# Kernel tuning notes

Measured on AMD Instinct MI355X. Metric: run time of the kernel, lower is better.

Reference implementation:

```python
import jax, jax.numpy as jnp
import numpy as np

NUM_NODES = 15000


def _gcn_conv(x, W, b, src, dst, norm, num_nodes):
    # PyG GCNConv: x' = D^-1/2 (A + I) D^-1/2 (x W) + b
    h = x @ W                                   # [N, out]
    msg = h[src] * norm[:, None]                # gather + scale per edge
    out = jax.ops.segment_sum(msg, dst, num_segments=num_nodes)
    return out + b


def setup_inputs() -> dict:
    key = jax.random.key(0)
    ks = jax.random.split(key, 12)
    T = 100000
    E = 200000
    inp = {
        "x": jax.random.normal(ks[0], (NUM_NODES, 768), jnp.float32),
        "r_emb": jax.random.normal(ks[1], (T, 768), jnp.float32),
        "W1": jax.random.normal(ks[2], (768, 10), jnp.float32) * 0.05,
        "b1": jax.random.normal(ks[3], (10,), jnp.float32) * 0.05,
        "W2": jax.random.normal(ks[4], (10, 128), jnp.float32) * 0.05,
        "b2": jax.random.normal(ks[5], (128,), jnp.float32) * 0.05,
        "W_ih": jax.random.normal(ks[6], (512, 1024), jnp.float32) * 0.03,
        "W_hh": jax.random.normal(ks[7], (512, 128), jnp.float32) * 0.03,
        "b_ih": jax.random.normal(ks[8], (512,), jnp.float32) * 0.03,
        "b_hh": jax.random.normal(ks[9], (512,), jnp.float32) * 0.03,
        "edge_index": jax.random.randint(ks[10], (2, E), 0, NUM_NODES).astype(jnp.int64),
        "triples": jax.random.randint(ks[11], (T, 3), 0, NUM_NODES).astype(jnp.int64),
    }
    return inp


def reference(x, r_emb, W1, b1, W2, b2, W_ih, W_hh, b_ih, b_hh, edge_index, triples):
    N = x.shape[0]
    H = 128  # lstm hidden size
    # --- add self loops, symmetric GCN normalization ---
    loop = jnp.arange(N, dtype=edge_index.dtype)
    src = jnp.concatenate([edge_index[0], loop])
    dst = jnp.concatenate([edge_index[1], loop])
    deg = jax.ops.segment_sum(jnp.ones_like(dst, jnp.float32), dst, num_segments=N)
    dinv = jnp.where(deg > 0, jax.lax.rsqrt(deg), 0.0)
    norm = dinv[src] * dinv[dst]                      # [E+N]
    # --- 2-layer GCN ---
    h = jax.nn.relu(_gcn_conv(x, W1, b1, src, dst, norm, N))   # [N, 10]
    z = _gcn_conv(h, W2, b2, src, dst, norm, N)                # [N, 128]
    # --- per-triple LSTM scoring, batched (seq_len=1, zero init state) ---
    hvec = z[triples[:, 0]]                           # [T, 128]
    tvec = z[triples[:, 2]]                           # [T, 128]
    feat = jnp.concatenate([hvec, r_emb, tvec], axis=-1)       # [T, 1024]
    gates = feat @ W_ih.T + (b_ih + b_hh)             # [T, 512]; h0=0 so W_hh term vanishes
    i_g, f_g, g_g, o_g = jnp.split(gates, 4, axis=-1)  # torch gate order i,f,g,o
    c = jax.nn.sigmoid(i_g) * jnp.tanh(g_g)           # c0 = 0 -> forget term drops
    out = jax.nn.sigmoid(o_g) * jnp.tanh(c)           # [T, 128]
    score = jax.nn.sigmoid(jnp.sum(out, axis=-1))     # [T]
    return score
```

## Files before the change

### kernel.cpp

```cpp
#include <hip/hip_runtime.h>

#define NF 768
#define D1 10
#define D2 128
#define BM 64
#define NS 24

typedef __attribute__((ext_vector_type(8))) short bf16x8;
typedef __attribute__((ext_vector_type(16))) float f32x16;

static __device__ __forceinline__ float sigf(float v){ return 1.0f/(1.0f+__expf(-v)); }
static __device__ __forceinline__ float tanhfast(float v){ return 2.0f/(1.0f+__expf(-2.0f*v)) - 1.0f; }
static __device__ __forceinline__ short f2bf(float f){
    unsigned u = __float_as_uint(f);
    u += 0x7fffu + ((u>>16)&1u);
    return (short)(u>>16);
}
static __device__ __forceinline__ float bf2f(ushort h){
    return __uint_as_float(((unsigned)h)<<16);
}

__global__ void k_deg(const int* __restrict__ dst, int* __restrict__ cnt, int E){
    int e = blockIdx.x*256 + threadIdx.x;
    if(e<E) atomicAdd(&cnt[dst[e]], 1);
}
__global__ void k_dinv(const int* __restrict__ cnt, float* __restrict__ dinv, int N){
    int n = blockIdx.x*256 + threadIdx.x;
    if(n<N) dinv[n] = rsqrtf((float)cnt[n] + 1.0f);
}

__global__ __launch_bounds__(256) void k_scan(const int* __restrict__ cnt,
                                              int* __restrict__ rowptr,
                                              int* __restrict__ rowcur, int N, int E){
    __shared__ int part[256];
    int t = threadIdx.x;
    int C = (N+255)/256;
    int lo = t*C, hi = lo+C; if(hi>N) hi=N; if(lo>N) lo=N;
    int s=0;
    for(int i=lo;i<hi;i++) s += cnt[i];
    part[t]=s;
    __syncthreads();
    if(t==0){
        int run=0;
        for(int i=0;i<256;i++){ int v=part[i]; part[i]=run; run+=v; }
        rowptr[N]=E;
    }
    __syncthreads();
    int run = part[t];
    for(int i=lo;i<hi;i++){ rowptr[i]=run; rowcur[i]=run; run += cnt[i]; }
}

__global__ void k_fill(const int* __restrict__ src, const int* __restrict__ dst,
                       const float* __restrict__ dinv, int* __restrict__ rowcur,
                       int* __restrict__ esrc, float* __restrict__ enorm, int E){
    int e = blockIdx.x*256 + threadIdx.x;
    if(e>=E) return;
    int s=src[e], d=dst[e];
    int pos = atomicAdd(&rowcur[d], 1);
    esrc[pos]=s;
    enorm[pos]=dinv[s]*dinv[d];
}

__global__ __launch_bounds__(256) void k_h1(const float* __restrict__ x,
                                            const float* __restrict__ W1,
                                            float* __restrict__ h1, int N){
    __shared__ float w1s[NF*D1];
    for(int i=threadIdx.x;i<NF*D1;i+=256) w1s[i]=W1[i];
    __syncthreads();
    int row = blockIdx.x*4 + (threadIdx.x>>6);
    int lane = threadIdx.x&63;
    if(row>=N) return;
    const float* xr = x + (size_t)row*NF;
    float acc[D1];
#pragma unroll
    for(int c=0;c<D1;c++) acc[c]=0.f;
#pragma unroll
    for(int i=0;i<NF/64;i++){
        float xa = xr[lane+64*i];
        const float* w = &w1s[(lane+64*i)*D1];
#pragma unroll
        for(int c=0;c<D1;c++) acc[c] += xa*w[c];
    }
#pragma unroll
    for(int c=0;c<D1;c++){
        float v=acc[c];
#pragma unroll
        for(int off=32;off;off>>=1) v += __shfl_down(v,off,64);
        if(lane==0) h1[(size_t)row*D1+c]=v;
    }
}

__global__ void k_scat1(const int* __restrict__ src, const int* __restrict__ dst,
                        const float* __restrict__ dinv, const float* __restrict__ h1,
                        float* __restrict__ agg1, int E){
    int gid = blockIdx.x*256 + threadIdx.x;
    if(gid >= E*D1) return;
    int e = gid/D1, c = gid - e*D1;
    int s = src[e], d = dst[e];
    float norm = dinv[s]*dinv[d];
    atomicAdd(&agg1[(size_t)d*D1+c], h1[(size_t)s*D1+c]*norm);
}

__global__ void k_relu(float* __restrict__ agg1, const float* __restrict__ h1,
                       const float* __restrict__ dinv, const float* __restrict__ b1, int N){
    int gid = blockIdx.x*256 + threadIdx.x;
    if(gid >= N*D1) return;
    int n = gid/D1, c = gid - n*D1;
    float di = dinv[n];
    float v = agg1[gid] + h1[gid]*di*di + b1[c];
    agg1[gid] = v>0.f ? v : 0.f;
}

__global__ __launch_bounds__(128) void k_hz(const float* __restrict__ h,
                                            const float* __restrict__ W2,
                                            float* __restrict__ hz, int N){
    __shared__ float w2s[D1*D2];
    int j = threadIdx.x;
    for(int i=j;i<D1*D2;i+=128) w2s[i]=W2[i];
    __syncthreads();
    int n = blockIdx.x;
    if(n>=N) return;
    const float* hr = h + (size_t)n*D1;
    float acc=0.f;
#pragma unroll
    for(int k=0;k<D1;k++) acc += hr[k]*w2s[k*D2+j];
    hz[(size_t)n*D2+j]=acc;
}

__global__ __launch_bounds__(128) void k_gath2(const float* __restrict__ hz,
        const int* __restrict__ rowptr, const int* __restrict__ esrc,
        const float* __restrict__ enorm, const float* __restrict__ dinv,
        const float* __restrict__ b2, float* __restrict__ z, int N){
    int n = blockIdx.x;
    int c = threadIdx.x;
    int e0 = rowptr[n], e1 = rowptr[n+1];
    float di = dinv[n];
    float acc = hz[(size_t)n*D2+c]*di*di + b2[c];
    int e = e0;
    for(; e+1<e1; e+=2){
        int s0=esrc[e], s1=esrc[e+1];
        float w0=enorm[e], w1=enorm[e+1];
        acc += hz[(size_t)s0*D2+c]*w0 + hz[(size_t)s1*D2+c]*w1;
    }
    if(e<e1) acc += hz[(size_t)esrc[e]*D2+c]*enorm[e];
    z[(size_t)n*D2+c]=acc;
}

__global__ void k_wimgB(const float* __restrict__ Wih, ushort* __restrict__ img){
    int gid = blockIdx.x*256 + threadIdx.x;
    if(gid >= 12*48*64) return;
    int l = gid & 63;
    int ks16 = (gid>>6) % 48;
    int f = gid / (48*64);
    int dd = l & 31, kb = l>>5;
    int wn = f/3, gi = f - wn*3;
    int gbase = (gi==0)?0:((gi==1)?256:384);
    int wrow = gbase + wn*32 + dd;
    int k = ks16*16 + kb*8;
    const float* p = Wih + (size_t)wrow*1024 + 128 + k;
    float4 v0=*(const float4*)p, v1=*(const float4*)(p+4);
    bf16x8 o;
    o[0]=f2bf(v0.x); o[1]=f2bf(v0.y); o[2]=f2bf(v0.z); o[3]=f2bf(v0.w);
    o[4]=f2bf(v1.x); o[5]=f2bf(v1.y); o[6]=f2bf(v1.z); o[7]=f2bf(v1.w);
    *(bf16x8*)(img + (size_t)gid*8) = o;
}

__global__ void k_wimgZ(const float* __restrict__ Wih, ushort* __restrict__ img){
    int gid = blockIdx.x*256 + threadIdx.x;
    if(gid >= 24*8*64) return;
    int l = gid & 63;
    int ks16 = (gid>>6) & 7;
    int f = gid >> 9;
    int j = f*32 + (l&31);
    int kb = l>>5;
    int k = ks16*16 + kb*8;
    int jq = (j<384)? j : j-384;
    int wrow = (jq<128)? jq : jq+128;
    int wcol = (j<384)? k : (896+k);
    const float* p = Wih + (size_t)wrow*1024 + wcol;
    float4 v0=*(const float4*)p, v1=*(const float4*)(p+4);
    bf16x8 o;
    o[0]=f2bf(v0.x); o[1]=f2bf(v0.y); o[2]=f2bf(v0.z); o[3]=f2bf(v0.w);
    o[4]=f2bf(v1.x); o[5]=f2bf(v1.y); o[6]=f2bf(v1.z); o[7]=f2bf(v1.w);
    *(bf16x8*)(img + (size_t)gid*8) = o;
}

__global__ __launch_bounds__(256) void k_zw_m(const float* __restrict__ z,
                                              const ushort* __restrict__ img,
                                              ushort* __restrict__ zwht, int N){
    __shared__ ushort As[8*64*8];
    int tid=threadIdx.x, lane=tid&63, w=tid>>6;
    int n0 = blockIdx.x*32;
#pragma unroll
    for(int i=0;i<2;i++){
        int s = tid + 256*i;
        int ks16 = s>>6, l = s&63;
        int row = l&31, kb=l>>5;
        int n = n0+row; if(n>=N) n=N-1;
        const float* p = z + (size_t)n*D2 + ks16*16 + kb*8;
        float4 v0=*(const float4*)p, v1=*(const float4*)(p+4);
        bf16x8 o;
        o[0]=f2bf(v0.x); o[1]=f2bf(v0.y); o[2]=f2bf(v0.z); o[3]=f2bf(v0.w);
        o[4]=f2bf(v1.x); o[5]=f2bf(v1.y); o[6]=f2bf(v1.z); o[7]=f2bf(v1.w);
        *(bf16x8*)(&As[(size_t)s*8]) = o;
    }
    __syncthreads();
    f32x16 acc[6];
    const f32x16 zer = {0,0,0,0,0,0,0,0,0,0,0,0,0,0,0,0};
#pragma unroll
    for(int nf=0;nf<6;nf++) acc[nf]=zer;
#pragma unroll
    for(int ks16=0;ks16<8;ks16++){
        bf16x8 a = *(const bf16x8*)&As[(ks16*64+lane)*8];
#pragma unroll
        for(int nf=0;nf<6;nf++){
            int f = w*6+nf;
            bf16x8 b = *(const bf16x8*)(img + ((size_t)(f*8+ks16)*64 + lane)*8);
            acc[nf] = __builtin_amdgcn_mfma_f32_32x32x16_bf16(a,b,acc[nf],0,0,0);
        }
    }
    int l31=lane&31, lh=lane>>5;
#pragma unroll
    for(int nf=0;nf<6;nf++){
        int j = (w*6+nf)*32 + l31;
#pragma unroll
        for(int r=0;r<16;r++){
            int row = (r&3)+8*(r>>2)+4*lh;
            int n = n0+row;
            if(n<N) zwht[(size_t)n*768 + j] = (ushort)f2bf(acc[nf][r]);
        }
    }
}

__global__ __launch_bounds__(256,3) void k_big(
    const float* __restrict__ remb, const ushort* __restrict__ img,
    const ushort* __restrict__ zwht, const float* __restrict__ b_ih,
    const float* __restrict__ b_hh, const int* __restrict__ trip,
    float* __restrict__ score, int T)
{
    __shared__ ushort As[2][4*64*8];
    __shared__ float rowsum[BM];
    __shared__ int sh_th[BM], sh_tt[BM];
    int tid=threadIdx.x, lane=tid&63, wn=tid>>6;
    int l31=lane&31, lh=lane>>5;
    int t0 = blockIdx.x*BM;
    if(tid<BM){
        rowsum[tid]=0.f;
        int t=t0+tid, tc=(t<T)?t:T-1;
        sh_th[tid]=trip[3*tc]; sh_tt[tid]=trip[3*tc+2];
    }
    const int arow=(tid&7)+8*(tid>>5);
    const int akb=(tid>>3)&1, akh=(tid>>4)&1;
    const int aslot = (((arow>>5)*2+akh)*64 + (arow&31)+32*akb)*8;
    const size_t arowg = (size_t)((t0+arow<T)?(t0+arow):(T-1))*NF + akb*8 + akh*16;
    const ushort* wbase = img + ((size_t)(wn*3)*48*64 + lane)*8;

    float4 p0a,p0b,p1a,p1b;
    p0a=*(const float4*)(remb+arowg);      p0b=*(const float4*)(remb+arowg+4);
    p1a=*(const float4*)(remb+arowg+32);   p1b=*(const float4*)(remb+arowg+36);

    f32x16 acc[2][3];
    const f32x16 zer = {0,0,0,0,0,0,0,0,0,0,0,0,0,0,0,0};
#pragma unroll
    for(int m=0;m<2;m++)
#pragma unroll
        for(int g=0;g<3;g++) acc[m][g]=zer;

#define STAGE(B,VA,VB) { bf16x8 o_; \
    o_[0]=f2bf(VA.x); o_[1]=f2bf(VA.y); o_[2]=f2bf(VA.z); o_[3]=f2bf(VA.w); \
    o_[4]=f2bf(VB.x); o_[5]=f2bf(VB.y); o_[6]=f2bf(VB.z); o_[7]=f2bf(VB.w); \
    *(bf16x8*)(&As[B][aslot]) = o_; }

#define COMPUTE(B,KS) { \
    _Pragma("unroll") \
    for(int kh=0;kh<2;kh++){ \
        bf16x8 a0 = *(const bf16x8*)&As[B][((0*2+kh)*64+lane)*8]; \
        bf16x8 a1 = *(const bf16x8*)&As[B][((1*2+kh)*64+lane)*8]; \
        int ksh = (KS)*2+kh; \
        bf16x8 b0 = *(const bf16x8*)(wbase + (size_t)(0*48+ksh)*512); \
        bf16x8 b1 = *(const bf16x8*)(wbase + (size_t)(1*48+ksh)*512); \
        bf16x8 b2v= *(const bf16x8*)(wbase + (size_t)(2*48+ksh)*512); \
        acc[0][0]=__builtin_amdgcn_mfma_f32_32x32x16_bf16(a0,b0 ,acc[0][0],0,0,0); \
        acc[0][1]=__builtin_amdgcn_mfma_f32_32x32x16_bf16(a0,b1 ,acc[0][1],0,0,0); \
        acc[0][2]=__builtin_amdgcn_mfma_f32_32x32x16_bf16(a0,b2v,acc[0][2],0,0,0); \
        acc[1][0]=__builtin_amdgcn_mfma_f32_32x32x16_bf16(a1,b0 ,acc[1][0],0,0,0); \
        acc[1][1]=__builtin_amdgcn_mfma_f32_32x32x16_bf16(a1,b1 ,acc[1][1],0,0,0); \
        acc[1][2]=__builtin_amdgcn_mfma_f32_32x32x16_bf16(a1,b2v,acc[1][2],0,0,0); \
    } }

    STAGE(0, p0a, p0b);
    __syncthreads();

    for(int ks=0; ks<NS; ks+=2){
        if(ks+2<NS){
            p0a=*(const float4*)(remb+arowg+(size_t)(ks+2)*32);
            p0b=*(const float4*)(remb+arowg+(size_t)(ks+2)*32+4);
        }
        STAGE(1, p1a, p1b);
        COMPUTE(0, ks);
        __syncthreads();
        if(ks+3<NS){
            p1a=*(const float4*)(remb+arowg+(size_t)(ks+3)*32);
            p1b=*(const float4*)(remb+arowg+(size_t)(ks+3)*32+4);
        }
        if(ks+2<NS){ STAGE(0, p0a, p0b); }
        COMPUTE(1, ks+1);
        __syncthreads();
    }

    int d = wn*32+l31;
    float bi=b_ih[d]+b_hh[d];
    float bg=b_ih[256+d]+b_hh[256+d];
    float bo=b_ih[384+d]+b_hh[384+d];
#pragma unroll
    for(int m=0;m<2;m++){
#pragma unroll
        for(int r=0;r<16;r++){
            int row = m*32 + (r&3)+8*(r>>2)+4*lh;
            int t = t0+row;
            float ov = 0.f;
            if(t<T){
                const ushort* zh = zwht + (size_t)sh_th[row]*768;
                const ushort* zt = zwht + (size_t)sh_tt[row]*768 + 384;
                float ig = acc[m][0][r] + bf2f(zh[d])     + bf2f(zt[d])     + bi;
                float gg = acc[m][1][r] + bf2f(zh[128+d]) + bf2f(zt[128+d]) + bg;
                float og = acc[m][2][r] + bf2f(zh[256+d]) + bf2f(zt[256+d]) + bo;
                float cc = sigf(ig)*tanhfast(gg);
                ov = sigf(og)*tanhfast(cc);
            }
#pragma unroll
            for(int off=1; off<32; off<<=1) ov += __shfl_xor(ov, off, 64);
            if(l31==0) atomicAdd(&rowsum[row], ov);
        }
    }
    __syncthreads();
    if(tid < BM){
        int t = t0 + tid;
        if(t < T) score[t] = sigf(rowsum[tid]);
    }
#undef STAGE
#undef COMPUTE
}

extern "C" void kernel_launch(void* const* d_in, const int* in_sizes, int n_in,
                              void* d_out, int out_size, void* d_ws, size_t ws_size,
                              hipStream_t stream){
    const float* x    = (const float*)d_in[0];
    const float* remb = (const float*)d_in[1];
    const float* W1   = (const float*)d_in[2];
    const float* b1   = (const float*)d_in[3];
    const float* W2   = (const float*)d_in[4];
    const float* b2   = (const float*)d_in[5];
    const float* Wih  = (const float*)d_in[6];
    const float* b_ih = (const float*)d_in[8];
    const float* b_hh = (const float*)d_in[9];
    const int*   ei   = (const int*)d_in[10];
    const int*   trip = (const int*)d_in[11];
    float* score = (float*)d_out;

    const int N = in_sizes[0]/NF;
    const int E = in_sizes[10]/2;
    const int T = in_sizes[11]/3;
    const int* src = ei;
    const int* dst = ei + E;

    float* ws = (float*)d_ws;
    size_t o = 0;
    ushort* WimgB = (ushort*)(ws+o); o += 12*48*64*8/2;
    ushort* WimgZ = (ushort*)(ws+o); o += 24*8*64*8/2;
    ushort* zwht  = (ushort*)(ws+o); o += (size_t)N*768/2;
    int*   cnt    = (int*)(ws+o);    o += (size_t)((N+8)&~7);
    int*   rowptr = (int*)(ws+o);    o += (size_t)((N+8)&~7);
    int*   rowcur = (int*)(ws+o);    o += (size_t)((N+8)&~7);
    int*   esrc   = (int*)(ws+o);    o += (size_t)E;
    float* enorm  = ws+o;            o += (size_t)E;
    float* dinv   = ws+o;            o += (size_t)((N+7)&~7);
    float* h1     = ws+o;            o += (size_t)N*D1;
    float* agg1   = ws+o;            o += (size_t)N*D1;
    float* hz     = ws+o;            o += (size_t)N*D2;
    float* z      = ws+o;            o += (size_t)N*D2;
    (void)ws_size; (void)n_in; (void)out_size;

    hipMemsetAsync(cnt, 0, (size_t)N*sizeof(int), stream);
    hipMemsetAsync(agg1, 0, (size_t)N*D1*sizeof(float), stream);

    k_wimgB<<<dim3((12*48*64+255)/256), dim3(256), 0, stream>>>(Wih, WimgB);
    k_wimgZ<<<dim3((24*8*64+255)/256),  dim3(256), 0, stream>>>(Wih, WimgZ);
    k_deg  <<<dim3((E+255)/256), dim3(256), 0, stream>>>(dst, cnt, E);
    k_dinv <<<dim3((N+255)/256), dim3(256), 0, stream>>>(cnt, dinv, N);
    k_scan <<<dim3(1), dim3(256), 0, stream>>>(cnt, rowptr, rowcur, N, E);
    k_fill <<<dim3((E+255)/256), dim3(256), 0, stream>>>(src, dst, dinv, rowcur, esrc, enorm, E);
    k_h1   <<<dim3((N+3)/4), dim3(256), 0, stream>>>(x, W1, h1, N);
    k_scat1<<<dim3((E*D1+255)/256), dim3(256), 0, stream>>>(src, dst, dinv, h1, agg1, E);
    k_relu <<<dim3((N*D1+255)/256), dim3(256), 0, stream>>>(agg1, h1, dinv, b1, N);
    k_hz   <<<dim3(N), dim3(128), 0, stream>>>(agg1, W2, hz, N);
    k_gath2<<<dim3(N), dim3(128), 0, stream>>>(hz, rowptr, esrc, enorm, dinv, b2, z, N);
    k_zw_m <<<dim3((N+31)/32), dim3(256), 0, stream>>>(z, WimgZ, zwht, N);
    k_big  <<<dim3((T+BM-1)/BM), dim3(256), 0, stream>>>(remb, WimgB, zwht, b_ih, b_hh, trip, score, T);
}
```

Baseline: 363.0 us.

## Fold z·W_ih head/tail projection into main MFMA GEMM and restructure GCN layer one

The precomputed per-node z·W_ih table (k_zw_m, k_wimgZ) is removed. The main triple kernel now gathers bf16 z rows for head and tail and runs them as extra K-steps in its MFMA GEMM over the full 1024-wide input. That GEMM no longer stages through LDS: each lane loads A fragments directly from global memory into a register-prefetch pipeline, and __launch_bounds__ drops the occupancy hint. Layer one's atomic scatter plus ReLU pass is replaced by a CSR gather kernel, dinv is folded into the scan, and k_h1 reads x as float4 against a transposed W1. This removes the large zwht intermediate and several launches, at the cost of extra per-triple MFMA work and uncoalesced direct global A-fragment loads.

```diff
diff --git a/kernel.cpp b/kernel.cpp
--- a/kernel.cpp
+++ b/kernel.cpp
@@ -4,7 +4,6 @@
 #define D1 10
 #define D2 128
 #define BM 64
-#define NS 24
 
 typedef __attribute__((ext_vector_type(8))) short bf16x8;
 typedef __attribute__((ext_vector_type(16))) float f32x16;
@@ -16,22 +15,15 @@
     u += 0x7fffu + ((u>>16)&1u);
     return (short)(u>>16);
 }
-static __device__ __forceinline__ float bf2f(ushort h){
-    return __uint_as_float(((unsigned)h)<<16);
-}
 
 __global__ void k_deg(const int* __restrict__ dst, int* __restrict__ cnt, int E){
     int e = blockIdx.x*256 + threadIdx.x;
     if(e<E) atomicAdd(&cnt[dst[e]], 1);
 }
-__global__ void k_dinv(const int* __restrict__ cnt, float* __restrict__ dinv, int N){
-    int n = blockIdx.x*256 + threadIdx.x;
-    if(n<N) dinv[n] = rsqrtf((float)cnt[n] + 1.0f);
-}
 
 __global__ __launch_bounds__(256) void k_scan(const int* __restrict__ cnt,
-                                              int* __restrict__ rowptr,
-                                              int* __restrict__ rowcur, int N, int E){
+                                              int* __restrict__ rowptr, int* __restrict__ rowcur,
+                                              float* __restrict__ dinv, int N, int E){
     __shared__ int part[256];
     int t = threadIdx.x;
     int C = (N+255)/256;
@@ -47,7 +39,10 @@
     }
     __syncthreads();
     int run = part[t];
-    for(int i=lo;i<hi;i++){ rowptr[i]=run; rowcur[i]=run; run += cnt[i]; }
+    for(int i=lo;i<hi;i++){
+        rowptr[i]=run; rowcur[i]=run; run += cnt[i];
+        dinv[i] = rsqrtf((float)cnt[i] + 1.0f);
+    }
 }
 
 __global__ void k_fill(const int* __restrict__ src, const int* __restrict__ dst,
@@ -64,51 +59,78 @@
 __global__ __launch_bounds__(256) void k_h1(const float* __restrict__ x,
                                             const float* __restrict__ W1,
                                             float* __restrict__ h1, int N){
-    __shared__ float w1s[NF*D1];
-    for(int i=threadIdx.x;i<NF*D1;i+=256) w1s[i]=W1[i];
+    __shared__ float wt[D1*NF];
+    for(int idx=threadIdx.x; idx<NF*D1; idx+=256){
+        int k=idx/D1, c=idx-k*D1;
+        wt[c*NF+k]=W1[idx];
+    }
     __syncthreads();
     int row = blockIdx.x*4 + (threadIdx.x>>6);
     int lane = threadIdx.x&63;
     if(row>=N) return;
-    const float* xr = x + (size_t)row*NF;
+    const float4* xr = (const float4*)(x + (size_t)row*NF);
     float acc[D1];
 #pragma unroll
     for(int c=0;c<D1;c++) acc[c]=0.f;
 #pragma unroll
-    for(int i=0;i<NF/64;i++){
-        float xa = xr[lane+64*i];
-        const float* w = &w1s[(lane+64*i)*D1];
-#pragma unroll
-        for(int c=0;c<D1;c++) acc[c] += xa*w[c];
+    for(int i=0;i<3;i++){
+        float4 v = xr[lane + 64*i];
+#pragma unroll
+        for(int c=0;c<D1;c++){
+            float4 w = *(const float4*)&wt[c*NF + (lane+64*i)*4];
+            acc[c] += v.x*w.x + v.y*w.y + v.z*w.z + v.w*w.w;
+        }
     }
 #pragma unroll
     for(int c=0;c<D1;c++){
         float v=acc[c];
 #pragma unroll
         for(int off=32;off;off>>=1) v += __shfl_down(v,off,64);
-        if(lane==0) h1[(size_t)row*D1+c]=v;
-    }
-}
-
-__global__ void k_scat1(const int* __restrict__ src, const int* __restrict__ dst,
-                        const float* __restrict__ dinv, const float* __restrict__ h1,
-                        float* __restrict__ agg1, int E){
-    int gid = blockIdx.x*256 + threadIdx.x;
-    if(gid >= E*D1) return;
-    int e = gid/D1, c = gid - e*D1;
-    int s = src[e], d = dst[e];
-    float norm = dinv[s]*dinv[d];
-    atomicAdd(&agg1[(size_t)d*D1+c], h1[(size_t)s*D1+c]*norm);
-}
-
-__global__ void k_relu(float* __restrict__ agg1, const float* __restrict__ h1,
-                       const float* __restrict__ dinv, const float* __restrict__ b1, int N){
-    int gid = blockIdx.x*256 + threadIdx.x;
-    if(gid >= N*D1) return;
-    int n = gid/D1, c = gid - n*D1;
-    float di = dinv[n];
-    float v = agg1[gid] + h1[gid]*di*di + b1[c];
-    agg1[gid] = v>0.f ? v : 0.f;
+        acc[c]=v;
+    }
+    if(lane==0){
+#pragma unroll
+        for(int c=0;c<D1;c++) h1[(size_t)row*D1+c]=acc[c];
+    }
+}
+
+__global__ __launch_bounds__(256) void k_gath1(const float* __restrict__ h1,
+        const int* __restrict__ rowptr, const int* __restrict__ esrc,
+        const float* __restrict__ enorm, const float* __restrict__ dinv,
+        const float* __restrict__ b1, float* __restrict__ h, int N){
+    int node = blockIdx.x*4 + (threadIdx.x>>6);
+    int lane = threadIdx.x&63;
+    if(node>=N) return;
+    int e0=rowptr[node], e1=rowptr[node+1];
+    float acc[D1];
+#pragma unroll
+    for(int c=0;c<D1;c++) acc[c]=0.f;
+    for(int e=e0+lane; e<e1; e+=64){
+        int s=esrc[e]; float w=enorm[e];
+        const float* hr = h1 + (size_t)s*D1;
+#pragma unroll
+        for(int c=0;c<D1;c++) acc[c] += hr[c]*w;
+    }
+    if(lane==0){
+        float di=dinv[node], d2=di*di;
+        const float* hr = h1 + (size_t)node*D1;
+#pragma unroll
+        for(int c=0;c<D1;c++) acc[c] += hr[c]*d2;
+    }
+#pragma unroll
+    for(int c=0;c<D1;c++){
+        float v=acc[c];
+#pragma unroll
+        for(int off=32;off;off>>=1) v += __shfl_down(v,off,64);
+        acc[c]=v;
+    }
+    if(lane==0){
+#pragma unroll
+        for(int c=0;c<D1;c++){
+            float v = acc[c] + b1[c];
+            h[(size_t)node*D1+c] = v>0.f ? v : 0.f;
+        }
+    }
 }
 
 __global__ __launch_bounds__(128) void k_hz(const float* __restrict__ h,
@@ -130,7 +152,7 @@
 __global__ __launch_bounds__(128) void k_gath2(const float* __restrict__ hz,
         const int* __restrict__ rowptr, const int* __restrict__ esrc,
         const float* __restrict__ enorm, const float* __restrict__ dinv,
-        const float* __restrict__ b2, float* __restrict__ z, int N){
+        const float* __restrict__ b2, ushort* __restrict__ zb, int N){
     int n = blockIdx.x;
     int c = threadIdx.x;
     int e0 = rowptr[n], e1 = rowptr[n+1];
@@ -143,21 +165,21 @@
         acc += hz[(size_t)s0*D2+c]*w0 + hz[(size_t)s1*D2+c]*w1;
     }
     if(e<e1) acc += hz[(size_t)esrc[e]*D2+c]*enorm[e];
-    z[(size_t)n*D2+c]=acc;
+    zb[(size_t)n*D2+c] = (ushort)f2bf(acc);
 }
 
 __global__ void k_wimgB(const float* __restrict__ Wih, ushort* __restrict__ img){
     int gid = blockIdx.x*256 + threadIdx.x;
-    if(gid >= 12*48*64) return;
+    if(gid >= 12*64*64) return;
     int l = gid & 63;
-    int ks16 = (gid>>6) % 48;
-    int f = gid / (48*64);
+    int ks16 = (gid>>6) & 63;
+    int f = gid >> 12;
     int dd = l & 31, kb = l>>5;
     int wn = f/3, gi = f - wn*3;
     int gbase = (gi==0)?0:((gi==1)?256:384);
     int wrow = gbase + wn*32 + dd;
     int k = ks16*16 + kb*8;
-    const float* p = Wih + (size_t)wrow*1024 + 128 + k;
+    const float* p = Wih + (size_t)wrow*1024 + k;
     float4 v0=*(const float4*)p, v1=*(const float4*)(p+4);
     bf16x8 o;
     o[0]=f2bf(v0.x); o[1]=f2bf(v0.y); o[2]=f2bf(v0.z); o[3]=f2bf(v0.w);
@@ -165,99 +187,32 @@
     *(bf16x8*)(img + (size_t)gid*8) = o;
 }
 
-__global__ void k_wimgZ(const float* __restrict__ Wih, ushort* __restrict__ img){
-    int gid = blockIdx.x*256 + threadIdx.x;
-    if(gid >= 24*8*64) return;
-    int l = gid & 63;
-    int ks16 = (gid>>6) & 7;
-    int f = gid >> 9;
-    int j = f*32 + (l&31);
-    int kb = l>>5;
-    int k = ks16*16 + kb*8;
-    int jq = (j<384)? j : j-384;
-    int wrow = (jq<128)? jq : jq+128;
-    int wcol = (j<384)? k : (896+k);
-    const float* p = Wih + (size_t)wrow*1024 + wcol;
-    float4 v0=*(const float4*)p, v1=*(const float4*)(p+4);
-    bf16x8 o;
-    o[0]=f2bf(v0.x); o[1]=f2bf(v0.y); o[2]=f2bf(v0.z); o[3]=f2bf(v0.w);
-    o[4]=f2bf(v1.x); o[5]=f2bf(v1.y); o[6]=f2bf(v1.z); o[7]=f2bf(v1.w);
-    *(bf16x8*)(img + (size_t)gid*8) = o;
-}
-
-__global__ __launch_bounds__(256) void k_zw_m(const float* __restrict__ z,
-                                              const ushort* __restrict__ img,
-                                              ushort* __restrict__ zwht, int N){
-    __shared__ ushort As[8*64*8];
-    int tid=threadIdx.x, lane=tid&63, w=tid>>6;
-    int n0 = blockIdx.x*32;
-#pragma unroll
-    for(int i=0;i<2;i++){
-        int s = tid + 256*i;
-        int ks16 = s>>6, l = s&63;
-        int row = l&31, kb=l>>5;
-        int n = n0+row; if(n>=N) n=N-1;
-        const float* p = z + (size_t)n*D2 + ks16*16 + kb*8;
-        float4 v0=*(const float4*)p, v1=*(const float4*)(p+4);
-        bf16x8 o;
-        o[0]=f2bf(v0.x); o[1]=f2bf(v0.y); o[2]=f2bf(v0.z); o[3]=f2bf(v0.w);
-        o[4]=f2bf(v1.x); o[5]=f2bf(v1.y); o[6]=f2bf(v1.z); o[7]=f2bf(v1.w);
-        *(bf16x8*)(&As[(size_t)s*8]) = o;
-    }
-    __syncthreads();
-    f32x16 acc[6];
-    const f32x16 zer = {0,0,0,0,0,0,0,0,0,0,0,0,0,0,0,0};
-#pragma unroll
-    for(int nf=0;nf<6;nf++) acc[nf]=zer;
-#pragma unroll
-    for(int ks16=0;ks16<8;ks16++){
-        bf16x8 a = *(const bf16x8*)&As[(ks16*64+lane)*8];
-#pragma unroll
-        for(int nf=0;nf<6;nf++){
-            int f = w*6+nf;
-            bf16x8 b = *(const bf16x8*)(img + ((size_t)(f*8+ks16)*64 + lane)*8);
-            acc[nf] = __builtin_amdgcn_mfma_f32_32x32x16_bf16(a,b,acc[nf],0,0,0);
-        }
-    }
-    int l31=lane&31, lh=lane>>5;
-#pragma unroll
-    for(int nf=0;nf<6;nf++){
-        int j = (w*6+nf)*32 + l31;
-#pragma unroll
-        for(int r=0;r<16;r++){
-            int row = (r&3)+8*(r>>2)+4*lh;
-            int n = n0+row;
-            if(n<N) zwht[(size_t)n*768 + j] = (ushort)f2bf(acc[nf][r]);
-        }
-    }
-}
-
-__global__ __launch_bounds__(256,3) void k_big(
+__global__ __launch_bounds__(256) void k_big(
     const float* __restrict__ remb, const ushort* __restrict__ img,
-    const ushort* __restrict__ zwht, const float* __restrict__ b_ih,
+    const ushort* __restrict__ zb, const float* __restrict__ b_ih,
     const float* __restrict__ b_hh, const int* __restrict__ trip,
     float* __restrict__ score, int T)
 {
-    __shared__ ushort As[2][4*64*8];
     __shared__ float rowsum[BM];
-    __shared__ int sh_th[BM], sh_tt[BM];
     int tid=threadIdx.x, lane=tid&63, wn=tid>>6;
     int l31=lane&31, lh=lane>>5;
-    int t0 = blockIdx.x*BM;
-    if(tid<BM){
-        rowsum[tid]=0.f;
-        int t=t0+tid, tc=(t<T)?t:T-1;
-        sh_th[tid]=trip[3*tc]; sh_tt[tid]=trip[3*tc+2];
-    }
-    const int arow=(tid&7)+8*(tid>>5);
-    const int akb=(tid>>3)&1, akh=(tid>>4)&1;
-    const int aslot = (((arow>>5)*2+akh)*64 + (arow&31)+32*akb)*8;
-    const size_t arowg = (size_t)((t0+arow<T)?(t0+arow):(T-1))*NF + akb*8 + akh*16;
-    const ushort* wbase = img + ((size_t)(wn*3)*48*64 + lane)*8;
-
-    float4 p0a,p0b,p1a,p1b;
-    p0a=*(const float4*)(remb+arowg);      p0b=*(const float4*)(remb+arowg+4);
-    p1a=*(const float4*)(remb+arowg+32);   p1b=*(const float4*)(remb+arowg+36);
+    int t0=blockIdx.x*BM;
+    if(tid<BM) rowsum[tid]=0.f;
+    __syncthreads();
+
+    int th[2], tt[2];
+    size_t rbase[2];
+#pragma unroll
+    for(int m=0;m<2;m++){
+        int t = t0 + l31 + m*32; if(t>=T) t=T-1;
+        rbase[m] = (size_t)t*NF;
+        th[m]=trip[3*t]; tt[m]=trip[3*t+2];
+    }
+    const float* ra0 = remb + rbase[0] + lh*8;
+    const float* ra1 = remb + rbase[1] + lh*8;
+    const ushort* wb0 = img + ((size_t)(wn*3+0)*64*64 + lane)*8;
+    const ushort* wb1 = img + ((size_t)(wn*3+1)*64*64 + lane)*8;
+    const ushort* wb2 = img + ((size_t)(wn*3+2)*64*64 + lane)*8;
 
     f32x16 acc[2][3];
     const f32x16 zer = {0,0,0,0,0,0,0,0,0,0,0,0,0,0,0,0};
@@ -266,47 +221,83 @@
 #pragma unroll
         for(int g=0;g<3;g++) acc[m][g]=zer;
 
-#define STAGE(B,VA,VB) { bf16x8 o_; \
-    o_[0]=f2bf(VA.x); o_[1]=f2bf(VA.y); o_[2]=f2bf(VA.z); o_[3]=f2bf(VA.w); \
-    o_[4]=f2bf(VB.x); o_[5]=f2bf(VB.y); o_[6]=f2bf(VB.z); o_[7]=f2bf(VB.w); \
-    *(bf16x8*)(&As[B][aslot]) = o_; }
-
-#define COMPUTE(B,KS) { \
-    _Pragma("unroll") \
-    for(int kh=0;kh<2;kh++){ \
-        bf16x8 a0 = *(const bf16x8*)&As[B][((0*2+kh)*64+lane)*8]; \
-        bf16x8 a1 = *(const bf16x8*)&As[B][((1*2+kh)*64+lane)*8]; \
-        int ksh = (KS)*2+kh; \
-        bf16x8 b0 = *(const bf16x8*)(wbase + (size_t)(0*48+ksh)*512); \
-        bf16x8 b1 = *(const bf16x8*)(wbase + (size_t)(1*48+ksh)*512); \
-        bf16x8 b2v= *(const bf16x8*)(wbase + (size_t)(2*48+ksh)*512); \
-        acc[0][0]=__builtin_amdgcn_mfma_f32_32x32x16_bf16(a0,b0 ,acc[0][0],0,0,0); \
-        acc[0][1]=__builtin_amdgcn_mfma_f32_32x32x16_bf16(a0,b1 ,acc[0][1],0,0,0); \
-        acc[0][2]=__builtin_amdgcn_mfma_f32_32x32x16_bf16(a0,b2v,acc[0][2],0,0,0); \
-        acc[1][0]=__builtin_amdgcn_mfma_f32_32x32x16_bf16(a1,b0 ,acc[1][0],0,0,0); \
-        acc[1][1]=__builtin_amdgcn_mfma_f32_32x32x16_bf16(a1,b1 ,acc[1][1],0,0,0); \
-        acc[1][2]=__builtin_amdgcn_mfma_f32_32x32x16_bf16(a1,b2v,acc[1][2],0,0,0); \
-    } }
-
-    STAGE(0, p0a, p0b);
-    __syncthreads();
-
-    for(int ks=0; ks<NS; ks+=2){
-        if(ks+2<NS){
-            p0a=*(const float4*)(remb+arowg+(size_t)(ks+2)*32);
-            p0b=*(const float4*)(remb+arowg+(size_t)(ks+2)*32+4);
-        }
-        STAGE(1, p1a, p1b);
-        COMPUTE(0, ks);
-        __syncthreads();
-        if(ks+3<NS){
-            p1a=*(const float4*)(remb+arowg+(size_t)(ks+3)*32);
-            p1b=*(const float4*)(remb+arowg+(size_t)(ks+3)*32+4);
-        }
-        if(ks+2<NS){ STAGE(0, p0a, p0b); }
-        COMPUTE(1, ks+1);
-        __syncthreads();
-    }
+#define CVT(d_, va_, vb_) { \
+    d_[0]=f2bf(va_.x); d_[1]=f2bf(va_.y); d_[2]=f2bf(va_.z); d_[3]=f2bf(va_.w); \
+    d_[4]=f2bf(vb_.x); d_[5]=f2bf(vb_.y); d_[6]=f2bf(vb_.z); d_[7]=f2bf(vb_.w); }
+
+    float4 pa[4][2][2];
+    bf16x8 pb[2][3];
+#pragma unroll
+    for(int p=0;p<4;p++){
+        pa[p][0][0]=*(const float4*)(ra0+p*16); pa[p][0][1]=*(const float4*)(ra0+p*16+4);
+        pa[p][1][0]=*(const float4*)(ra1+p*16); pa[p][1][1]=*(const float4*)(ra1+p*16+4);
+    }
+#pragma unroll
+    for(int p=0;p<2;p++){
+        pb[p][0]=*(const bf16x8*)(wb0+(size_t)(p+8)*512);
+        pb[p][1]=*(const bf16x8*)(wb1+(size_t)(p+8)*512);
+        pb[p][2]=*(const bf16x8*)(wb2+(size_t)(p+8)*512);
+    }
+    for(int g0=0; g0<48; g0+=8){
+#pragma unroll
+        for(int i=0;i<8;i++){
+            int g = g0+i;
+            int s = i&3, bs = i&1;
+            bf16x8 a0, a1;
+            CVT(a0, pa[s][0][0], pa[s][0][1]);
+            CVT(a1, pa[s][1][0], pa[s][1][1]);
+            bf16x8 b0=pb[bs][0], b1=pb[bs][1], b2=pb[bs][2];
+            int ga = g+4; if(ga>47) ga=47;
+            pa[s][0][0]=*(const float4*)(ra0+ga*16); pa[s][0][1]=*(const float4*)(ra0+ga*16+4);
+            pa[s][1][0]=*(const float4*)(ra1+ga*16); pa[s][1][1]=*(const float4*)(ra1+ga*16+4);
+            int gb = g+2; if(gb>47) gb=47;
+            pb[bs][0]=*(const bf16x8*)(wb0+(size_t)(gb+8)*512);
+            pb[bs][1]=*(const bf16x8*)(wb1+(size_t)(gb+8)*512);
+            pb[bs][2]=*(const bf16x8*)(wb2+(size_t)(gb+8)*512);
+            acc[0][0]=__builtin_amdgcn_mfma_f32_32x32x16_bf16(a0,b0,acc[0][0],0,0,0);
+            acc[0][1]=__builtin_amdgcn_mfma_f32_32x32x16_bf16(a0,b1,acc[0][1],0,0,0);
+            acc[0][2]=__builtin_amdgcn_mfma_f32_32x32x16_bf16(a0,b2,acc[0][2],0,0,0);
+            acc[1][0]=__builtin_amdgcn_mfma_f32_32x32x16_bf16(a1,b0,acc[1][0],0,0,0);
+            acc[1][1]=__builtin_amdgcn_mfma_f32_32x32x16_bf16(a1,b1,acc[1][1],0,0,0);
+            acc[1][2]=__builtin_amdgcn_mfma_f32_32x32x16_bf16(a1,b2,acc[1][2],0,0,0);
+        }
+    }
+
+    const ushort* za[2] = { zb + (size_t)th[0]*D2 + lh*8, zb + (size_t)th[1]*D2 + lh*8 };
+    const ushort* zc[2] = { zb + (size_t)tt[0]*D2 + lh*8, zb + (size_t)tt[1]*D2 + lh*8 };
+#define ZLD(m_,j_) ( (j_)<8 ? *(const bf16x8*)(za[m_]+(j_)*16) : *(const bf16x8*)(zc[m_]+((j_)-8)*16) )
+#define ZIMG(j_) ( (j_)<8 ? (j_) : (j_)+48 )
+    bf16x8 pz[4][2];
+    bf16x8 qb[2][3];
+#pragma unroll
+    for(int p=0;p<4;p++){ pz[p][0]=ZLD(0,p); pz[p][1]=ZLD(1,p); }
+#pragma unroll
+    for(int p=0;p<2;p++){
+        qb[p][0]=*(const bf16x8*)(wb0+(size_t)ZIMG(p)*512);
+        qb[p][1]=*(const bf16x8*)(wb1+(size_t)ZIMG(p)*512);
+        qb[p][2]=*(const bf16x8*)(wb2+(size_t)ZIMG(p)*512);
+    }
+#pragma unroll
+    for(int j=0;j<16;j++){
+        int s=j&3, bs=j&1;
+        bf16x8 a0=pz[s][0], a1=pz[s][1];
+        bf16x8 b0=qb[bs][0], b1=qb[bs][1], b2=qb[bs][2];
+        if(j+4<16){ pz[s][0]=ZLD(0,j+4); pz[s][1]=ZLD(1,j+4); }
+        if(j+2<16){
+            qb[bs][0]=*(const bf16x8*)(wb0+(size_t)ZIMG(j+2)*512);
+            qb[bs][1]=*(const bf16x8*)(wb1+(size_t)ZIMG(j+2)*512);
+            qb[bs][2]=*(const bf16x8*)(wb2+(size_t)ZIMG(j+2)*512);
+        }
+        acc[0][0]=__builtin_amdgcn_mfma_f32_32x32x16_bf16(a0,b0,acc[0][0],0,0,0);
+        acc[0][1]=__builtin_amdgcn_mfma_f32_32x32x16_bf16(a0,b1,acc[0][1],0,0,0);
+        acc[0][2]=__builtin_amdgcn_mfma_f32_32x32x16_bf16(a0,b2,acc[0][2],0,0,0);
+        acc[1][0]=__builtin_amdgcn_mfma_f32_32x32x16_bf16(a1,b0,acc[1][0],0,0,0);
+        acc[1][1]=__builtin_amdgcn_mfma_f32_32x32x16_bf16(a1,b1,acc[1][1],0,0,0);
+        acc[1][2]=__builtin_amdgcn_mfma_f32_32x32x16_bf16(a1,b2,acc[1][2],0,0,0);
+    }
+#undef ZLD
+#undef ZIMG
+#undef CVT
 
     int d = wn*32+l31;
     float bi=b_ih[d]+b_hh[d];
@@ -317,17 +308,11 @@
 #pragma unroll
         for(int r=0;r<16;r++){
             int row = m*32 + (r&3)+8*(r>>2)+4*lh;
-            int t = t0+row;
-            float ov = 0.f;
-            if(t<T){
-                const ushort* zh = zwht + (size_t)sh_th[row]*768;
-                const ushort* zt = zwht + (size_t)sh_tt[row]*768 + 384;
-                float ig = acc[m][0][r] + bf2f(zh[d])     + bf2f(zt[d])     + bi;
-                float gg = acc[m][1][r] + bf2f(zh[128+d]) + bf2f(zt[128+d]) + bg;
-                float og = acc[m][2][r] + bf2f(zh[256+d]) + bf2f(zt[256+d]) + bo;
-                float cc = sigf(ig)*tanhfast(gg);
-                ov = sigf(og)*tanhfast(cc);
-            }
+            float ig = acc[m][0][r] + bi;
+            float gg = acc[m][1][r] + bg;
+            float og = acc[m][2][r] + bo;
+            float cc = sigf(ig)*tanhfast(gg);
+            float ov = sigf(og)*tanhfast(cc);
 #pragma unroll
             for(int off=1; off<32; off<<=1) ov += __shfl_xor(ov, off, 64);
             if(l31==0) atomicAdd(&rowsum[row], ov);
@@ -338,8 +323,6 @@
         int t = t0 + tid;
         if(t < T) score[t] = sigf(rowsum[tid]);
     }
-#undef STAGE
-#undef COMPUTE
 }
 
 extern "C" void kernel_launch(void* const* d_in, const int* in_sizes, int n_in,
@@ -366,35 +349,28 @@
 
     float* ws = (float*)d_ws;
     size_t o = 0;
-    ushort* WimgB = (ushort*)(ws+o); o += 12*48*64*8/2;
-    ushort* WimgZ = (ushort*)(ws+o); o += 24*8*64*8/2;
-    ushort* zwht  = (ushort*)(ws+o); o += (size_t)N*768/2;
-    int*   cnt    = (int*)(ws+o);    o += (size_t)((N+8)&~7);
-    int*   rowptr = (int*)(ws+o);    o += (size_t)((N+8)&~7);
-    int*   rowcur = (int*)(ws+o);    o += (size_t)((N+8)&~7);
-    int*   esrc   = (int*)(ws+o);    o += (size_t)E;
-    float* enorm  = ws+o;            o += (size_t)E;
-    float* dinv   = ws+o;            o += (size_t)((N+7)&~7);
-    float* h1     = ws+o;            o += (size_t)N*D1;
-    float* agg1   = ws+o;            o += (size_t)N*D1;
-    float* hz     = ws+o;            o += (size_t)N*D2;
-    float* z      = ws+o;            o += (size_t)N*D2;
+    ushort* img  = (ushort*)(ws+o); o += (size_t)12*64*64*8/2;
+    ushort* zb   = (ushort*)(ws+o); o += (size_t)N*D2/2;
+    int*   cnt    = (int*)(ws+o);   o += (size_t)((N+8)&~7);
+    int*   rowptr = (int*)(ws+o);   o += (size_t)((N+8)&~7);
+    int*   rowcur = (int*)(ws+o);   o += (size_t)((N+8)&~7);
+    int*   esrc   = (int*)(ws+o);   o += (size_t)E;
+    float* enorm  = ws+o;           o += (size_t)E;
+    float* dinv   = ws+o;           o += (size_t)((N+7)&~7);
+    float* h1     = ws+o;           o += (size_t)N*D1;
+    float* hbuf   = ws+o;           o += (size_t)N*D1;
+    float* hz     = ws+o;           o += (size_t)N*D2;
     (void)ws_size; (void)n_in; (void)out_size;
 
     hipMemsetAsync(cnt, 0, (size_t)N*sizeof(int), stream);
-    hipMemsetAsync(agg1, 0, (size_t)N*D1*sizeof(float), stream);
-
-    k_wimgB<<<dim3((12*48*64+255)/256), dim3(256), 0, stream>>>(Wih, WimgB);
-    k_wimgZ<<<dim3((24*8*64+255)/256),  dim3(256), 0, stream>>>(Wih, WimgZ);
+
+    k_wimgB<<<dim3((12*64*64+255)/256), dim3(256), 0, stream>>>(Wih, img);
     k_deg  <<<dim3((E+255)/256), dim3(256), 0, stream>>>(dst, cnt, E);
-    k_dinv <<<dim3((N+255)/256), dim3(256), 0, stream>>>(cnt, dinv, N);
-    k_scan <<<dim3(1), dim3(256), 0, stream>>>(cnt, rowptr, rowcur, N, E);
+    k_scan <<<dim3(1), dim3(256), 0, stream>>>(cnt, rowptr, rowcur, dinv, N, E);
     k_fill <<<dim3((E+255)/256), dim3(256), 0, stream>>>(src, dst, dinv, rowcur, esrc, enorm, E);
     k_h1   <<<dim3((N+3)/4), dim3(256), 0, stream>>>(x, W1, h1, N);
-    k_scat1<<<dim3((E*D1+255)/256), dim3(256), 0, stream>>>(src, dst, dinv, h1, agg1, E);
-    k_relu <<<dim3((N*D1+255)/256), dim3(256), 0, stream>>>(agg1, h1, dinv, b1, N);
-    k_hz   <<<dim3(N), dim3(128), 0, stream>>>(agg1, W2, hz, N);
-    k_gath2<<<dim3(N), dim3(128), 0, stream>>>(hz, rowptr, esrc, enorm, dinv, b2, z, N);
-    k_zw_m <<<dim3((N+31)/32), dim3(256), 0, stream>>>(z, WimgZ, zwht, N);
-    k_big  <<<dim3((T+BM-1)/BM), dim3(256), 0, stream>>>(remb, WimgB, zwht, b_ih, b_hh, trip, score, T);
-}
+    k_gath1<<<dim3((N+3)/4), dim3(256), 0, stream>>>(h1, rowptr, esrc, enorm, dinv, b1, hbuf, N);
+    k_hz   <<<dim3(N), dim3(128), 0, stream>>>(hbuf, W2, hz, N);
+    k_gath2<<<dim3(N), dim3(128), 0, stream>>>(hz, rowptr, esrc, enorm, dinv, b2, zb, N);
+    k_big  <<<dim3((T+BM-1)/BM), dim3(256), 0, stream>>>(remb, img, zb, b_ih, b_hh, trip, score, T);
+}
```

Result: slower. 684.1 us (+88.4%).
